# Optimization experiments

Hardware: AMD Instinct MI355X
Metric: run time of the kernel (lower is better)

The kernel has to match this reference:

```python
import jax, jax.numpy as jnp
import numpy as np

Q_HEADS, KV_HEADS, DIMS = 16, 4, 1024
HEAD_DIM = DIMS // Q_HEADS          # 64
GROUPS = Q_HEADS // KV_HEADS        # 4


def rope(x):
    # x: [..., s, d]; base-10 thetas, positions start at 1 (per source RoPE)
    s, d = x.shape[-2], x.shape[-1]
    thetas = 10.0 ** (-jnp.arange(d // 2, dtype=jnp.float32))
    angles = jnp.arange(1, s + 1, dtype=jnp.float32)[:, None] * thetas  # [s, d/2]
    cos, sin = jnp.cos(angles), jnp.sin(angles)
    xr, xi = x[..., ::2], x[..., 1::2]
    outr = xr * cos - xi * sin
    outi = xr * sin + xi * cos
    return jnp.stack([outr, outi], axis=-1).reshape(x.shape)  # re-interleave


def setup_inputs() -> dict:
    key = jax.random.key(0)
    ks = jax.random.split(key, 5)
    b, s, in_dim = 4, 2048, 1024
    q = jax.random.normal(ks[0], (b, s, in_dim), dtype=jnp.float32)
    mask = jnp.tril(jnp.ones((s, s), dtype=jnp.float32))  # 1 = keep, 0 = masked
    sc = 1.0 / np.sqrt(in_dim)
    Wq = jax.random.normal(ks[1], (in_dim, Q_HEADS, HEAD_DIM), dtype=jnp.float32) * sc
    Wk = jax.random.normal(ks[2], (in_dim, KV_HEADS, HEAD_DIM), dtype=jnp.float32) * sc
    Wv = jax.random.normal(ks[3], (in_dim, KV_HEADS, HEAD_DIM), dtype=jnp.float32) * sc
    Wo = jax.random.normal(ks[4], (KV_HEADS * HEAD_DIM, in_dim), dtype=jnp.float32) * (1.0 / np.sqrt(KV_HEADS * HEAD_DIM))
    return {"q": q, "mask": mask, "Wq": Wq, "Wk": Wk, "Wv": Wv, "Wo": Wo}


def reference(q, mask, Wq, Wk, Wv, Wo):
    b, s, in_dim = q.shape
    # projections (DenseGeneral, no bias)
    qh = jnp.einsum('bsi,ihd->bshd', q, Wq)   # [b, s, 16, 64]
    kh = jnp.einsum('bsi,ihd->bshd', q, Wk)   # [b, s, 4, 64]  (kv = q)
    vh = jnp.einsum('bsi,ihd->bshd', q, Wv)
    # '... s (h g) d -> ... g h s d' with g=GROUPS
    qh = qh.reshape(b, s, KV_HEADS, GROUPS, HEAD_DIM).transpose(0, 3, 2, 1, 4)  # [b,g,h,s,d]
    kh = kh.transpose(0, 2, 1, 3)  # [b, h, s, d]
    vh = vh.transpose(0, 2, 1, 3)
    qh = rope(qh)
    kh = rope(kh)
    # NOTE: source einsum sums over group axis g
    scores = jnp.einsum('bghsd,bhad->bhsa', qh, kh)  # [b, h, s, s]
    scores = scores - (1.0 / mask - 1.0)             # mask==0 -> -inf
    attn = jax.nn.softmax(scores / jnp.float32(HEAD_DIM ** 0.5), axis=-1)
    out = jnp.einsum('bhsa,bhad->bhsd', attn, vh)    # [b, h, s, d]
    out = out.transpose(0, 2, 1, 3).reshape(b, s, KV_HEADS * HEAD_DIM)
    return out @ Wo  # [b, s, in_dim]
```

## Files before the change

kernel.cpp:

```cpp
#include <hip/hip_runtime.h>
#include <math.h>

#define BATCH 4
#define SEQ   2048
#define DIN   1024
#define KVH   4
#define HD    64
#define MTOT  (BATCH*SEQ)
#define NPROJ 768
#define PROJ_STRIDE (BATCH*KVH*SEQ*HD)
#define NCHUNK_TOT 80

typedef unsigned short ushort_t;
typedef __attribute__((ext_vector_type(8))) short short8;
typedef __attribute__((ext_vector_type(4))) float f32x4;

#define QSCALE (0.125f * 1.44269504088896340736f)

__device__ inline ushort_t f2bf(float x) {
    union { float f; unsigned int u; } v; v.f = x;
    unsigned int r = v.u + 0x7fffu + ((v.u >> 16) & 1u);
    return (ushort_t)(r >> 16);
}
__device__ inline ushort_t f2bf_trunc(float x) {
    return (ushort_t)(__float_as_uint(x) >> 16);
}

__global__ __launch_bounds__(256) void prep_kernel(
        const float* __restrict__ Wq, const float* __restrict__ Wk,
        const float* __restrict__ Wv, const float* __restrict__ Wo,
        const float* __restrict__ X,
        ushort_t* __restrict__ Wcat_t, ushort_t* __restrict__ Wo_t,
        float2* __restrict__ ctab, ushort_t* __restrict__ Y) {
    const int bx = blockIdx.x;
    const int tid = threadIdx.x;
    if (bx < 4096) {
        int idx = bx * 256 + tid;
        if (idx < NPROJ * DIN) {
            int n = idx >> 10, k = idx & 1023;
            float v;
            if (n < 256) {
                const float* p = Wq + (size_t)k * 1024 + (n >> 6) * 256 + (n & 63);
                v = p[0] + p[64] + p[128] + p[192];
            } else if (n < 512) {
                v = Wk[(size_t)k * 256 + (n - 256)];
            } else {
                v = Wv[(size_t)k * 256 + (n - 512)];
            }
            Wcat_t[idx] = f2bf(v);
        } else {
            int t = idx - NPROJ * DIN;
            int n = t >> 8, k = t & 255;
            Wo_t[t] = f2bf(Wo[(size_t)k * 1024 + n]);
        }
    } else if (bx < 4352) {
        int t = (bx - 4096) * 256 + tid;
        int j = t & 31, s = t >> 5;
        float ang = (float)(s + 1) * exp10f(-(float)j);
        float sn, cs;
        sincosf(ang, &sn, &cs);
        ctab[t] = make_float2(cs, sn);
    } else {
        int i = ((bx - 4352) * 256 + tid) * 4;
        float4 v = *(const float4*)&X[i];
        ushort4 o;
        o.x = f2bf(v.x); o.y = f2bf(v.y); o.z = f2bf(v.z); o.w = f2bf(v.w);
        *(ushort4*)&Y[i] = o;
    }
}

template<int OUT_MODE>
__global__ __launch_bounds__(256) void gemm_mfma_kernel(
        const ushort_t* __restrict__ A, const ushort_t* __restrict__ Bt,
        float* __restrict__ Y, ushort_t* __restrict__ Qbf,
        ushort_t* __restrict__ Kbf, ushort_t* __restrict__ Vt,
        const float2* __restrict__ ctab, int K, int N) {
    __shared__ __align__(16) ushort_t As[128 * 64];
    __shared__ __align__(16) ushort_t Bs[64 * 64];
    const int tid  = threadIdx.x;
    const int w    = tid >> 6, lane = tid & 63;
    const int m15  = lane & 15, quad = lane >> 4;
    const int wm   = (w >> 1) * 64, wn = (w & 1) * 32;
    const int m0   = blockIdx.y * 128, n0 = blockIdx.x * 64;
    const int r8   = lane >> 3;
    const int c8   = (lane & 7) * 8;
    const int cs   = (((lane & 7) + r8) & 7) * 8;
    const int rotr = (m15 & 7) * 8;
    const int off0 = (quad * 8 + 64 - rotr) & 63;
    const int off1 = (32 + quad * 8 + 64 - rotr) & 63;

    const int niter = K >> 6;
    const int kst   = blockIdx.y & (niter - 1);

    f32x4 acc[4][2];
    #pragma unroll
    for (int i = 0; i < 4; ++i)
        #pragma unroll
        for (int j = 0; j < 2; ++j) acc[i][j] = (f32x4){0.f, 0.f, 0.f, 0.f};

    short8 ra[4], rb[2];
    {
        const int k0 = kst * 64;
        #pragma unroll
        for (int p = 0; p < 4; ++p)
            ra[p] = *(const short8*)(A + (size_t)(m0 + w * 32 + p * 8 + r8) * K + k0 + cs);
        #pragma unroll
        for (int p = 0; p < 2; ++p)
            rb[p] = *(const short8*)(Bt + (size_t)(n0 + w * 16 + p * 8 + r8) * K + k0 + cs);
    }

    for (int it = 0; it < niter; ++it) {
        __syncthreads();
        #pragma unroll
        for (int p = 0; p < 4; ++p)
            *(short8*)&As[(w * 32 + p * 8 + r8) * 64 + c8] = ra[p];
        #pragma unroll
        for (int p = 0; p < 2; ++p)
            *(short8*)&Bs[(w * 16 + p * 8 + r8) * 64 + c8] = rb[p];
        __syncthreads();

        if (it + 1 < niter) {
            const int kn = ((kst + it + 1) & (niter - 1)) * 64;
            #pragma unroll
            for (int p = 0; p < 4; ++p)
                ra[p] = *(const short8*)(A + (size_t)(m0 + w * 32 + p * 8 + r8) * K + kn + cs);
            #pragma unroll
            for (int p = 0; p < 2; ++p)
                rb[p] = *(const short8*)(Bt + (size_t)(n0 + w * 16 + p * 8 + r8) * K + kn + cs);
        }

        short8 af[4][2], bfm[2][2];
        #pragma unroll
        for (int i = 0; i < 4; ++i) {
            af[i][0] = *(const short8*)&As[(wm + i * 16 + m15) * 64 + off0];
            af[i][1] = *(const short8*)&As[(wm + i * 16 + m15) * 64 + off1];
        }
        #pragma unroll
        for (int j = 0; j < 2; ++j) {
            bfm[j][0] = *(const short8*)&Bs[(wn + j * 16 + m15) * 64 + off0];
            bfm[j][1] = *(const short8*)&Bs[(wn + j * 16 + m15) * 64 + off1];
        }
        #pragma unroll
        for (int i = 0; i < 4; ++i)
            #pragma unroll
            for (int j = 0; j < 2; ++j) {
                acc[i][j] = __builtin_amdgcn_mfma_f32_16x16x32_bf16(
                                af[i][0], bfm[j][0], acc[i][j], 0, 0, 0);
                acc[i][j] = __builtin_amdgcn_mfma_f32_16x16x32_bf16(
                                af[i][1], bfm[j][1], acc[i][j], 0, 0, 0);
            }
    }

    if (OUT_MODE == 0) {
        #pragma unroll
        for (int i = 0; i < 4; ++i)
            #pragma unroll
            for (int r = 0; r < 4; ++r) {
                size_t row = (size_t)(m0 + wm + i * 16 + quad * 4 + r);
                #pragma unroll
                for (int j = 0; j < 2; ++j)
                    Y[row * N + n0 + wn + j * 16 + m15] = acc[i][j][r];
            }
    } else {
        #pragma unroll
        for (int j = 0; j < 2; ++j) {
            int c = n0 + wn + j * 16 + m15;
            int proj = c >> 8, cc = c & 255;
            int hd = cc >> 6, d = cc & 63;
            if (proj < 2) {
                int jj = d >> 1;
                float sgn = (d & 1) ? 1.0f : -1.0f;
                float qs  = (proj == 0) ? QSCALE : 1.0f;
                ushort_t* dst = (proj ? Kbf : Qbf) + (size_t)hd * SEQ * HD + d;
                #pragma unroll
                for (int i = 0; i < 4; ++i)
                    #pragma unroll
                    for (int r = 0; r < 4; ++r) {
                        int m = m0 + wm + i * 16 + quad * 4 + r;
                        int b = m >> 11, s = m & (SEQ - 1);
                        float x = acc[i][j][r];
                        float p = __shfl_xor(x, 1);
                        float2 ct = ctab[s * 32 + jj];
                        float o = (x * ct.x + sgn * p * ct.y) * qs;
                        dst[(((size_t)b * KVH) * SEQ + s) * HD] = f2bf(o);
                    }
            } else {
                ushort_t* Vp = Vt + (((size_t)hd * HD) + d) * SEQ;
                #pragma unroll
                for (int i = 0; i < 4; ++i)
                    #pragma unroll
                    for (int r = 0; r < 4; ++r) {
                        int m = m0 + wm + i * 16 + quad * 4 + r;
                        int b = m >> 11, s = m & (SEQ - 1);
                        Vp[(size_t)b * KVH * HD * SEQ + s] = f2bf(acc[i][j][r]);
                    }
            }
        }
    }
}

__global__ __launch_bounds__(256) void attn_mfma_kernel(
        const ushort_t* __restrict__ Qbf, const ushort_t* __restrict__ Kbf,
        const ushort_t* __restrict__ Vtbf, float* __restrict__ pO,
        float* __restrict__ pL) {
    __shared__ __align__(16) ushort_t Ks[64][72];
    __shared__ __align__(16) ushort_t Vts[64][72];
    __shared__ __align__(16) ushort_t Ps[4][16][72];
    const int tid  = threadIdx.x;
    const int w    = tid >> 6, lane = tid & 63;
    const int m15  = lane & 15, quad = lane >> 4;
    const int bh   = blockIdx.y;
    const int f    = 79 - blockIdx.x;
    int qt, ch;
    if (f < 8)       { qt = f;                    ch = 0; }
    else if (f < 24) { qt = 8  + ((f - 8) >> 1);  ch = (f - 8) & 1; }
    else if (f < 48) { qt = 16 + (f - 24) / 3;    ch = (f - 24) % 3; }
    else             { qt = 24 + ((f - 48) >> 2); ch = (f - 48) & 3; }
    const int q0 = qt * 64;
    const int kt_beg = ch * 8;
    const int kt_end = min(kt_beg + 8, qt + 1);

    const ushort_t* Qb  = Qbf  + (size_t)bh * SEQ * HD;
    const ushort_t* Kb  = Kbf  + (size_t)bh * SEQ * HD;
    const ushort_t* Vtb = Vtbf + (size_t)bh * HD * SEQ;

    const int qrow = q0 + w * 16 + m15;
    short8 qf0 = *(const short8*)(Qb + (size_t)qrow * HD + quad * 8);
    short8 qf1 = *(const short8*)(Qb + (size_t)qrow * HD + 32 + quad * 8);

    f32x4 o[4];
    #pragma unroll
    for (int nt = 0; nt < 4; ++nt) o[nt] = (f32x4){0.f, 0.f, 0.f, 0.f};
    float lacc[4] = {0.f, 0.f, 0.f, 0.f};

    const int sc_ = tid & 7;
    const int sr_ = tid >> 3;

    short8 pk0, pk1, pv0, pv1;
    {
        const int k0 = kt_beg * 64;
        pk0 = *(const short8*)(Kb  + (size_t)(k0 + sr_) * HD + sc_ * 8);
        pk1 = *(const short8*)(Kb  + (size_t)(k0 + sr_ + 32) * HD + sc_ * 8);
        pv0 = *(const short8*)(Vtb + (size_t)sr_ * SEQ + k0 + sc_ * 8);
        pv1 = *(const short8*)(Vtb + (size_t)(sr_ + 32) * SEQ + k0 + sc_ * 8);
    }

    for (int kt = kt_beg; kt < kt_end; ++kt) {
        const int k0 = kt * 64;
        __syncthreads();
        *(short8*)&Ks[sr_][sc_*8]       = pk0;
        *(short8*)&Ks[sr_ + 32][sc_*8]  = pk1;
        *(short8*)&Vts[sr_][sc_*8]      = pv0;
        *(short8*)&Vts[sr_ + 32][sc_*8] = pv1;
        __syncthreads();

        if (kt + 1 < kt_end) {
            const int kn = k0 + 64;
            pk0 = *(const short8*)(Kb  + (size_t)(kn + sr_) * HD + sc_ * 8);
            pk1 = *(const short8*)(Kb  + (size_t)(kn + sr_ + 32) * HD + sc_ * 8);
            pv0 = *(const short8*)(Vtb + (size_t)sr_ * SEQ + kn + sc_ * 8);
            pv1 = *(const short8*)(Vtb + (size_t)(sr_ + 32) * SEQ + kn + sc_ * 8);
        }

        f32x4 sc4[4];
        #pragma unroll
        for (int nt = 0; nt < 4; ++nt) {
            f32x4 c = {0.f, 0.f, 0.f, 0.f};
            c = __builtin_amdgcn_mfma_f32_16x16x32_bf16(
                    qf0, *(const short8*)&Ks[nt*16 + m15][quad*8], c, 0, 0, 0);
            c = __builtin_amdgcn_mfma_f32_16x16x32_bf16(
                    qf1, *(const short8*)&Ks[nt*16 + m15][32 + quad*8], c, 0, 0, 0);
            sc4[nt] = c;
        }
        if (kt == qt) {
            #pragma unroll
            for (int nt = 0; nt < 4; ++nt) {
                int colg = k0 + nt*16 + m15;
                #pragma unroll
                for (int r = 0; r < 4; ++r) {
                    int rowg = q0 + w*16 + quad*4 + r;
                    if (colg > rowg) sc4[nt][r] = -INFINITY;
                }
            }
        }

        #pragma unroll
        for (int nt = 0; nt < 4; ++nt)
            #pragma unroll
            for (int r = 0; r < 4; ++r) {
                float e = exp2f(sc4[nt][r]);
                lacc[r] += e;
                Ps[w][quad*4 + r][nt*16 + m15] = f2bf_trunc(e);
            }

        short8 pa0 = *(const short8*)&Ps[w][m15][quad*8];
        short8 pa1 = *(const short8*)&Ps[w][m15][32 + quad*8];
        #pragma unroll
        for (int nt = 0; nt < 4; ++nt) {
            o[nt] = __builtin_amdgcn_mfma_f32_16x16x32_bf16(
                        pa0, *(const short8*)&Vts[nt*16 + m15][quad*8], o[nt], 0, 0, 0);
            o[nt] = __builtin_amdgcn_mfma_f32_16x16x32_bf16(
                        pa1, *(const short8*)&Vts[nt*16 + m15][32 + quad*8], o[nt], 0, 0, 0);
        }
    }

    const int blk = bh * NCHUNK_TOT + f;
    #pragma unroll
    for (int r = 0; r < 4; ++r) {
        float ls = lacc[r];
        ls += __shfl_xor(ls, 1);
        ls += __shfl_xor(ls, 2);
        ls += __shfl_xor(ls, 4);
        ls += __shfl_xor(ls, 8);
        int row = w * 16 + quad * 4 + r;
        if (m15 == 0) pL[(size_t)blk * 64 + row] = ls;
        #pragma unroll
        for (int nt = 0; nt < 4; ++nt)
            pO[(size_t)blk * 4096 + row * 64 + nt * 16 + m15] = o[nt][r];
    }
}

__device__ inline int flat_of(int qt, int ch) {
    if (qt < 8)  return qt;
    if (qt < 16) return 8 + (qt - 8) * 2 + ch;
    if (qt < 24) return 24 + (qt - 16) * 3 + ch;
    return 48 + (qt - 24) * 4 + ch;
}

__global__ __launch_bounds__(256) void combine_kernel(
        const float* __restrict__ pO, const float* __restrict__ pL,
        ushort_t* __restrict__ Out) {
    const int qt = blockIdx.x, bh = blockIdx.y;
    const int tid = threadIdx.x;
    const int row = tid >> 2;
    const int cb = (tid & 3) * 16;
    const int nch = (qt >> 3) + 1;
    float acc[16] = {};
    float lsum = 0.f;
    for (int c = 0; c < nch; ++c) {
        int blk = bh * NCHUNK_TOT + flat_of(qt, c);
        const float* po = pO + (size_t)blk * 4096 + row * 64 + cb;
        lsum += pL[(size_t)blk * 64 + row];
        #pragma unroll
        for (int j = 0; j < 4; ++j) {
            float4 v = *(const float4*)&po[j * 4];
            acc[j*4+0] += v.x; acc[j*4+1] += v.y;
            acc[j*4+2] += v.z; acc[j*4+3] += v.w;
        }
    }
    float inv = 1.0f / lsum;
    int b = bh >> 2, h = bh & 3;
    int s = qt * 64 + row;
    ushort_t tmp[16];
    #pragma unroll
    for (int j = 0; j < 16; ++j) tmp[j] = f2bf(acc[j] * inv);
    ushort_t* dst = Out + ((size_t)b * SEQ + s) * (KVH * HD) + h * HD + cb;
    *(uint4*)dst = ((uint4*)tmp)[0];
    *(uint4*)(dst + 8) = ((uint4*)tmp)[1];
}

extern "C" void kernel_launch(void* const* d_in, const int* in_sizes, int n_in,
                              void* d_out, int out_size, void* d_ws, size_t ws_size,
                              hipStream_t stream) {
    const float* q  = (const float*)d_in[0];
    const float* Wq = (const float*)d_in[2];
    const float* Wk = (const float*)d_in[3];
    const float* Wv = (const float*)d_in[4];
    const float* Wo = (const float*)d_in[5];
    float* out = (float*)d_out;

    char* base = (char*)d_ws;
    ushort_t* wcat_t  = (ushort_t*)(base);
    ushort_t* wo_t    = (ushort_t*)(base + 0x180000);
    float2*   ctab    = (float2*)(base + 0x200000);
    ushort_t* qin_bf  = (ushort_t*)(base + 0x280000);
    ushort_t* attn_bf = (ushort_t*)(base + 0x280000);
    float*    pO      = (float*)(base + 0x680000);
    float*    pL      = (float*)(base + 0x1A80000);
    ushort_t* q_bf    = (ushort_t*)(base + 0x1B00000);
    ushort_t* k_bf    = (ushort_t*)(base + 0x1F00000);
    ushort_t* vt_bf   = (ushort_t*)(base + 0x2300000);

    prep_kernel<<<12544, 256, 0, stream>>>(Wq, Wk, Wv, Wo, q,
                                           wcat_t, wo_t, ctab, qin_bf);

    dim3 gproj(NPROJ / 64, MTOT / 128);
    gemm_mfma_kernel<1><<<gproj, 256, 0, stream>>>(
        qin_bf, wcat_t, nullptr, q_bf, k_bf, vt_bf, ctab, DIN, NPROJ);

    dim3 gattn(NCHUNK_TOT, BATCH * KVH);
    attn_mfma_kernel<<<gattn, 256, 0, stream>>>(q_bf, k_bf, vt_bf, pO, pL);

    dim3 gcomb(SEQ / 64, BATCH * KVH);
    combine_kernel<<<gcomb, 256, 0, stream>>>(pO, pL, attn_bf);

    dim3 gout(DIN / 64, MTOT / 128);
    gemm_mfma_kernel<0><<<gout, 256, 0, stream>>>(
        attn_bf, wo_t, out, nullptr, nullptr, nullptr, nullptr, KVH * HD, DIN);
}
```

Measured before the change: 178.3 us.

## Fuse split-K combine into output projection and store partials in bf16

```diff
diff --git a/kernel.cpp b/kernel.cpp
--- a/kernel.cpp
+++ b/kernel.cpp
@@ -8,7 +8,6 @@
 #define HD    64
 #define MTOT  (BATCH*SEQ)
 #define NPROJ 768
-#define PROJ_STRIDE (BATCH*KVH*SEQ*HD)
 #define NCHUNK_TOT 80
 
 typedef unsigned short ushort_t;
@@ -24,6 +23,10 @@
 }
 __device__ inline ushort_t f2bf_trunc(float x) {
     return (ushort_t)(__float_as_uint(x) >> 16);
+}
+__device__ inline float bf2f(ushort_t x) {
+    union { unsigned int u; float f; } v; v.u = ((unsigned int)x) << 16;
+    return v.f;
 }
 
 __global__ __launch_bounds__(256) void prep_kernel(
@@ -69,12 +72,11 @@
     }
 }
 
-template<int OUT_MODE>
-__global__ __launch_bounds__(256) void gemm_mfma_kernel(
+__global__ __launch_bounds__(256) void proj_mfma_kernel(
         const ushort_t* __restrict__ A, const ushort_t* __restrict__ Bt,
-        float* __restrict__ Y, ushort_t* __restrict__ Qbf,
-        ushort_t* __restrict__ Kbf, ushort_t* __restrict__ Vt,
-        const float2* __restrict__ ctab, int K, int N) {
+        ushort_t* __restrict__ Qbf, ushort_t* __restrict__ Kbf,
+        ushort_t* __restrict__ Vt, const float2* __restrict__ ctab) {
+    const int K = DIN, N = NPROJ;
     __shared__ __align__(16) ushort_t As[128 * 64];
     __shared__ __align__(16) ushort_t Bs[64 * 64];
     const int tid  = threadIdx.x;
@@ -151,57 +153,45 @@
             }
     }
 
-    if (OUT_MODE == 0) {
-        #pragma unroll
-        for (int i = 0; i < 4; ++i)
-            #pragma unroll
-            for (int r = 0; r < 4; ++r) {
-                size_t row = (size_t)(m0 + wm + i * 16 + quad * 4 + r);
+    #pragma unroll
+    for (int j = 0; j < 2; ++j) {
+        int c = n0 + wn + j * 16 + m15;
+        int proj = c >> 8, cc = c & 255;
+        int hd = cc >> 6, d = cc & 63;
+        if (proj < 2) {
+            int jj = d >> 1;
+            float sgn = (d & 1) ? 1.0f : -1.0f;
+            float qs  = (proj == 0) ? QSCALE : 1.0f;
+            ushort_t* dst = (proj ? Kbf : Qbf) + (size_t)hd * SEQ * HD + d;
+            #pragma unroll
+            for (int i = 0; i < 4; ++i)
                 #pragma unroll
-                for (int j = 0; j < 2; ++j)
-                    Y[row * N + n0 + wn + j * 16 + m15] = acc[i][j][r];
-            }
-    } else {
-        #pragma unroll
-        for (int j = 0; j < 2; ++j) {
-            int c = n0 + wn + j * 16 + m15;
-            int proj = c >> 8, cc = c & 255;
-            int hd = cc >> 6, d = cc & 63;
-            if (proj < 2) {
-                int jj = d >> 1;
-                float sgn = (d & 1) ? 1.0f : -1.0f;
-                float qs  = (proj == 0) ? QSCALE : 1.0f;
-                ushort_t* dst = (proj ? Kbf : Qbf) + (size_t)hd * SEQ * HD + d;
+                for (int r = 0; r < 4; ++r) {
+                    int m = m0 + wm + i * 16 + quad * 4 + r;
+                    int b = m >> 11, s = m & (SEQ - 1);
+                    float x = acc[i][j][r];
+                    float p = __shfl_xor(x, 1);
+                    float2 ct = ctab[s * 32 + jj];
+                    float o = (x * ct.x + sgn * p * ct.y) * qs;
+                    dst[(((size_t)b * KVH) * SEQ + s) * HD] = f2bf(o);
+                }
+        } else {
+            ushort_t* Vp = Vt + (((size_t)hd * HD) + d) * SEQ;
+            #pragma unroll
+            for (int i = 0; i < 4; ++i)
                 #pragma unroll
-                for (int i = 0; i < 4; ++i)
-                    #pragma unroll
-                    for (int r = 0; r < 4; ++r) {
-                        int m = m0 + wm + i * 16 + quad * 4 + r;
-                        int b = m >> 11, s = m & (SEQ - 1);
-                        float x = acc[i][j][r];
-                        float p = __shfl_xor(x, 1);
-                        float2 ct = ctab[s * 32 + jj];
-                        float o = (x * ct.x + sgn * p * ct.y) * qs;
-                        dst[(((size_t)b * KVH) * SEQ + s) * HD] = f2bf(o);
-                    }
-            } else {
-                ushort_t* Vp = Vt + (((size_t)hd * HD) + d) * SEQ;
-                #pragma unroll
-                for (int i = 0; i < 4; ++i)
-                    #pragma unroll
-                    for (int r = 0; r < 4; ++r) {
-                        int m = m0 + wm + i * 16 + quad * 4 + r;
-                        int b = m >> 11, s = m & (SEQ - 1);
-                        Vp[(size_t)b * KVH * HD * SEQ + s] = f2bf(acc[i][j][r]);
-                    }
-            }
+                for (int r = 0; r < 4; ++r) {
+                    int m = m0 + wm + i * 16 + quad * 4 + r;
+                    int b = m >> 11, s = m & (SEQ - 1);
+                    Vp[(size_t)b * KVH * HD * SEQ + s] = f2bf(acc[i][j][r]);
+                }
         }
     }
 }
 
 __global__ __launch_bounds__(256) void attn_mfma_kernel(
         const ushort_t* __restrict__ Qbf, const ushort_t* __restrict__ Kbf,
-        const ushort_t* __restrict__ Vtbf, float* __restrict__ pO,
+        const ushort_t* __restrict__ Vtbf, ushort_t* __restrict__ pO,
         float* __restrict__ pL) {
     __shared__ __align__(16) ushort_t Ks[64][72];
     __shared__ __align__(16) ushort_t Vts[64][72];
@@ -316,7 +306,7 @@
         if (m15 == 0) pL[(size_t)blk * 64 + row] = ls;
         #pragma unroll
         for (int nt = 0; nt < 4; ++nt)
-            pO[(size_t)blk * 4096 + row * 64 + nt * 16 + m15] = o[nt][r];
+            pO[(size_t)blk * 4096 + row * 64 + nt * 16 + m15] = f2bf(o[nt][r]);
     }
 }
 
@@ -327,36 +317,84 @@
     return 48 + (qt - 24) * 4 + ch;
 }
 
-__global__ __launch_bounds__(256) void combine_kernel(
-        const float* __restrict__ pO, const float* __restrict__ pL,
-        ushort_t* __restrict__ Out) {
-    const int qt = blockIdx.x, bh = blockIdx.y;
-    const int tid = threadIdx.x;
-    const int row = tid >> 2;
-    const int cb = (tid & 3) * 16;
-    const int nch = (qt >> 3) + 1;
-    float acc[16] = {};
-    float lsum = 0.f;
-    for (int c = 0; c < nch; ++c) {
-        int blk = bh * NCHUNK_TOT + flat_of(qt, c);
-        const float* po = pO + (size_t)blk * 4096 + row * 64 + cb;
-        lsum += pL[(size_t)blk * 64 + row];
-        #pragma unroll
-        for (int j = 0; j < 4; ++j) {
-            float4 v = *(const float4*)&po[j * 4];
-            acc[j*4+0] += v.x; acc[j*4+1] += v.y;
-            acc[j*4+2] += v.z; acc[j*4+3] += v.w;
-        }
-    }
-    float inv = 1.0f / lsum;
-    int b = bh >> 2, h = bh & 3;
-    int s = qt * 64 + row;
-    ushort_t tmp[16];
+__global__ __launch_bounds__(256) void combine_outproj_kernel(
+        const ushort_t* __restrict__ pO, const float* __restrict__ pL,
+        const ushort_t* __restrict__ Wo_t, float* __restrict__ Out) {
+    __shared__ __align__(16) ushort_t As2[64 * 264];
+    __shared__ __align__(16) ushort_t Bs2[64 * 264];
+    const int tid  = threadIdx.x;
+    const int w    = tid >> 6, lane = tid & 63;
+    const int m15  = lane & 15, quad = lane >> 4;
+    const int b    = blockIdx.x >> 5;
+    const int qt   = blockIdx.x & 31;
+    const int nch  = (qt >> 3) + 1;
+
+    {
+        const int row = tid >> 2;
+        const int qtr = tid & 3;
+        #pragma unroll
+        for (int h = 0; h < 4; ++h) {
+            const int bh = b * KVH + h;
+            float acc[16] = {};
+            float lsum = 0.f;
+            for (int c = 0; c < nch; ++c) {
+                int blk = bh * NCHUNK_TOT + flat_of(qt, c);
+                const ushort_t* po = pO + (size_t)blk * 4096 + row * 64 + qtr * 16;
+                lsum += pL[(size_t)blk * 64 + row];
+                ushort_t raw[16];
+                *(uint4*)raw       = *(const uint4*)po;
+                *(uint4*)(raw + 8) = *(const uint4*)(po + 8);
+                #pragma unroll
+                for (int u = 0; u < 16; ++u) acc[u] += bf2f(raw[u]);
+            }
+            float inv = 1.0f / lsum;
+            ushort_t outv[16];
+            #pragma unroll
+            for (int u = 0; u < 16; ++u) outv[u] = f2bf(acc[u] * inv);
+            ushort_t* dst = &As2[row * 264 + h * 64 + qtr * 16];
+            *(uint4*)dst       = ((uint4*)outv)[0];
+            *(uint4*)(dst + 8) = ((uint4*)outv)[1];
+        }
+    }
+    __syncthreads();
+
+    short8 af2[8];
     #pragma unroll
-    for (int j = 0; j < 16; ++j) tmp[j] = f2bf(acc[j] * inv);
-    ushort_t* dst = Out + ((size_t)b * SEQ + s) * (KVH * HD) + h * HD + cb;
-    *(uint4*)dst = ((uint4*)tmp)[0];
-    *(uint4*)(dst + 8) = ((uint4*)tmp)[1];
+    for (int ks = 0; ks < 8; ++ks)
+        af2[ks] = *(const short8*)&As2[(w * 16 + m15) * 264 + ks * 32 + quad * 8];
+
+    const size_t outbase = ((size_t)b * SEQ + qt * 64 + w * 16) * DIN;
+
+    const int srow = tid >> 2;
+    const int sqtr = tid & 3;
+    for (int nc = 0; nc < 16; ++nc) {
+        const int n0 = nc * 64;
+        __syncthreads();
+        #pragma unroll
+        for (int u = 0; u < 8; ++u)
+            *(short8*)&Bs2[srow * 264 + sqtr * 64 + u * 8] =
+                *(const short8*)(Wo_t + (size_t)(n0 + srow) * 256 + sqtr * 64 + u * 8);
+        __syncthreads();
+
+        f32x4 acc2[4];
+        #pragma unroll
+        for (int j = 0; j < 4; ++j) acc2[j] = (f32x4){0.f, 0.f, 0.f, 0.f};
+        #pragma unroll
+        for (int ks = 0; ks < 8; ++ks) {
+            #pragma unroll
+            for (int j = 0; j < 4; ++j) {
+                short8 bfj = *(const short8*)&Bs2[(j * 16 + m15) * 264 + ks * 32 + quad * 8];
+                acc2[j] = __builtin_amdgcn_mfma_f32_16x16x32_bf16(
+                              af2[ks], bfj, acc2[j], 0, 0, 0);
+            }
+        }
+        #pragma unroll
+        for (int j = 0; j < 4; ++j)
+            #pragma unroll
+            for (int r = 0; r < 4; ++r)
+                Out[outbase + (size_t)(quad * 4 + r) * DIN + n0 + j * 16 + m15] =
+                    acc2[j][r];
+    }
 }
 
 extern "C" void kernel_launch(void* const* d_in, const int* in_sizes, int n_in,
@@ -374,8 +412,7 @@
     ushort_t* wo_t    = (ushort_t*)(base + 0x180000);
     float2*   ctab    = (float2*)(base + 0x200000);
     ushort_t* qin_bf  = (ushort_t*)(base + 0x280000);
-    ushort_t* attn_bf = (ushort_t*)(base + 0x280000);
-    float*    pO      = (float*)(base + 0x680000);
+    ushort_t* pO      = (ushort_t*)(base + 0x680000);
     float*    pL      = (float*)(base + 0x1A80000);
     ushort_t* q_bf    = (ushort_t*)(base + 0x1B00000);
     ushort_t* k_bf    = (ushort_t*)(base + 0x1F00000);
@@ -385,16 +422,11 @@
                                            wcat_t, wo_t, ctab, qin_bf);
 
     dim3 gproj(NPROJ / 64, MTOT / 128);
-    gemm_mfma_kernel<1><<<gproj, 256, 0, stream>>>(
-        qin_bf, wcat_t, nullptr, q_bf, k_bf, vt_bf, ctab, DIN, NPROJ);
+    proj_mfma_kernel<<<gproj, 256, 0, stream>>>(
+        qin_bf, wcat_t, q_bf, k_bf, vt_bf, ctab);
 
     dim3 gattn(NCHUNK_TOT, BATCH * KVH);
     attn_mfma_kernel<<<gattn, 256, 0, stream>>>(q_bf, k_bf, vt_bf, pO, pL);
 
-    dim3 gcomb(SEQ / 64, BATCH * KVH);
-    combine_kernel<<<gcomb, 256, 0, stream>>>(pO, pL, attn_bf);
-
-    dim3 gout(DIN / 64, MTOT / 128);
-    gemm_mfma_kernel<0><<<gout, 256, 0, stream>>>(
-        attn_bf, wo_t, out, nullptr, nullptr, nullptr, nullptr, KVH * HD, DIN);
-}
+    combine_outproj_kernel<<<MTOT / 64, 256, 0, stream>>>(pO, pL, wo_t, out);
+}
```

After: 198.6 us. 11.4% more time.

## Store attention partials in bf16 and remap blocks for XCD-aware locality

Applied to the files above, without the earlier changes.

```diff
diff --git a/kernel.cpp b/kernel.cpp
--- a/kernel.cpp
+++ b/kernel.cpp
@@ -8,7 +8,6 @@
 #define HD    64
 #define MTOT  (BATCH*SEQ)
 #define NPROJ 768
-#define PROJ_STRIDE (BATCH*KVH*SEQ*HD)
 #define NCHUNK_TOT 80
 
 typedef unsigned short ushort_t;
@@ -24,6 +23,10 @@
 }
 __device__ inline ushort_t f2bf_trunc(float x) {
     return (ushort_t)(__float_as_uint(x) >> 16);
+}
+__device__ inline float bf2f(ushort_t x) {
+    union { unsigned int u; float f; } v; v.u = ((unsigned int)x) << 16;
+    return v.f;
 }
 
 __global__ __launch_bounds__(256) void prep_kernel(
@@ -69,7 +72,7 @@
     }
 }
 
-template<int OUT_MODE>
+template<int OUT_MODE, int NTILES, int WORKS>
 __global__ __launch_bounds__(256) void gemm_mfma_kernel(
         const ushort_t* __restrict__ A, const ushort_t* __restrict__ Bt,
         float* __restrict__ Y, ushort_t* __restrict__ Qbf,
@@ -81,7 +84,10 @@
     const int w    = tid >> 6, lane = tid & 63;
     const int m15  = lane & 15, quad = lane >> 4;
     const int wm   = (w >> 1) * 64, wn = (w & 1) * 32;
-    const int m0   = blockIdx.y * 128, n0 = blockIdx.x * 64;
+    const int bid  = blockIdx.x;
+    const int work = (bid & 7) * WORKS + (bid >> 3);
+    const int mten = work / NTILES, nten = work - mten * NTILES;
+    const int m0   = mten * 128, n0 = nten * 64;
     const int r8   = lane >> 3;
     const int c8   = (lane & 7) * 8;
     const int cs   = (((lane & 7) + r8) & 7) * 8;
@@ -90,7 +96,7 @@
     const int off1 = (32 + quad * 8 + 64 - rotr) & 63;
 
     const int niter = K >> 6;
-    const int kst   = blockIdx.y & (niter - 1);
+    const int kst   = mten & (niter - 1);
 
     f32x4 acc[4][2];
     #pragma unroll
@@ -201,7 +207,7 @@
 
 __global__ __launch_bounds__(256) void attn_mfma_kernel(
         const ushort_t* __restrict__ Qbf, const ushort_t* __restrict__ Kbf,
-        const ushort_t* __restrict__ Vtbf, float* __restrict__ pO,
+        const ushort_t* __restrict__ Vtbf, ushort_t* __restrict__ pO,
         float* __restrict__ pL) {
     __shared__ __align__(16) ushort_t Ks[64][72];
     __shared__ __align__(16) ushort_t Vts[64][72];
@@ -209,8 +215,10 @@
     const int tid  = threadIdx.x;
     const int w    = tid >> 6, lane = tid & 63;
     const int m15  = lane & 15, quad = lane >> 4;
-    const int bh   = blockIdx.y;
-    const int f    = 79 - blockIdx.x;
+    const int bid  = blockIdx.x;
+    const int work = (bid & 7) * 160 + (bid >> 3);
+    const int bh   = work / 80;
+    const int f    = 79 - (work - bh * 80);
     int qt, ch;
     if (f < 8)       { qt = f;                    ch = 0; }
     else if (f < 24) { qt = 8  + ((f - 8) >> 1);  ch = (f - 8) & 1; }
@@ -316,7 +324,7 @@
         if (m15 == 0) pL[(size_t)blk * 64 + row] = ls;
         #pragma unroll
         for (int nt = 0; nt < 4; ++nt)
-            pO[(size_t)blk * 4096 + row * 64 + nt * 16 + m15] = o[nt][r];
+            pO[(size_t)blk * 4096 + row * 64 + nt * 16 + m15] = f2bf(o[nt][r]);
     }
 }
 
@@ -328,7 +336,7 @@
 }
 
 __global__ __launch_bounds__(256) void combine_kernel(
-        const float* __restrict__ pO, const float* __restrict__ pL,
+        const ushort_t* __restrict__ pO, const float* __restrict__ pL,
         ushort_t* __restrict__ Out) {
     const int qt = blockIdx.x, bh = blockIdx.y;
     const int tid = threadIdx.x;
@@ -339,14 +347,13 @@
     float lsum = 0.f;
     for (int c = 0; c < nch; ++c) {
         int blk = bh * NCHUNK_TOT + flat_of(qt, c);
-        const float* po = pO + (size_t)blk * 4096 + row * 64 + cb;
+        const ushort_t* po = pO + (size_t)blk * 4096 + row * 64 + cb;
         lsum += pL[(size_t)blk * 64 + row];
-        #pragma unroll
-        for (int j = 0; j < 4; ++j) {
-            float4 v = *(const float4*)&po[j * 4];
-            acc[j*4+0] += v.x; acc[j*4+1] += v.y;
-            acc[j*4+2] += v.z; acc[j*4+3] += v.w;
-        }
+        ushort_t raw[16];
+        *(uint4*)raw       = *(const uint4*)po;
+        *(uint4*)(raw + 8) = *(const uint4*)(po + 8);
+        #pragma unroll
+        for (int u = 0; u < 16; ++u) acc[u] += bf2f(raw[u]);
     }
     float inv = 1.0f / lsum;
     int b = bh >> 2, h = bh & 3;
@@ -375,7 +382,7 @@
     float2*   ctab    = (float2*)(base + 0x200000);
     ushort_t* qin_bf  = (ushort_t*)(base + 0x280000);
     ushort_t* attn_bf = (ushort_t*)(base + 0x280000);
-    float*    pO      = (float*)(base + 0x680000);
+    ushort_t* pO      = (ushort_t*)(base + 0x680000);
     float*    pL      = (float*)(base + 0x1A80000);
     ushort_t* q_bf    = (ushort_t*)(base + 0x1B00000);
     ushort_t* k_bf    = (ushort_t*)(base + 0x1F00000);
@@ -384,17 +391,14 @@
     prep_kernel<<<12544, 256, 0, stream>>>(Wq, Wk, Wv, Wo, q,
                                            wcat_t, wo_t, ctab, qin_bf);
 
-    dim3 gproj(NPROJ / 64, MTOT / 128);
-    gemm_mfma_kernel<1><<<gproj, 256, 0, stream>>>(
+    gemm_mfma_kernel<1, 12, 96><<<768, 256, 0, stream>>>(
         qin_bf, wcat_t, nullptr, q_bf, k_bf, vt_bf, ctab, DIN, NPROJ);
 
-    dim3 gattn(NCHUNK_TOT, BATCH * KVH);
-    attn_mfma_kernel<<<gattn, 256, 0, stream>>>(q_bf, k_bf, vt_bf, pO, pL);
+    attn_mfma_kernel<<<1280, 256, 0, stream>>>(q_bf, k_bf, vt_bf, pO, pL);
 
     dim3 gcomb(SEQ / 64, BATCH * KVH);
     combine_kernel<<<gcomb, 256, 0, stream>>>(pO, pL, attn_bf);
 
-    dim3 gout(DIN / 64, MTOT / 128);
-    gemm_mfma_kernel<0><<<gout, 256, 0, stream>>>(
+    gemm_mfma_kernel<0, 16, 128><<<1024, 256, 0, stream>>>(
         attn_bf, wo_t, out, nullptr, nullptr, nullptr, nullptr, KVH * HD, DIN);
 }
```

After: 172.6 us. -3.2%, faster.
